# Optimization experiments

Hardware: AMD Instinct MI355X
Metric: run time of the kernel (lower is better)

Reference implementation:

```python
import jax, jax.numpy as jnp
import numpy as np

# Single-device reference: with head-parallel world size 1, both _SeqAllToAll
# collectives are identities, so the forward is exactly the kv-packed causal
# attention computed by loongtrain_attn_kvpacked_func (flash-attn semantics).

def setup_inputs() -> dict:
    key = jax.random.key(0)
    k1, k2 = jax.random.split(key)
    B, S, H, D = 1, 2048, 32, 128
    q = jax.random.normal(k1, (B, S, H, D), dtype=jnp.float32)
    kv = jax.random.normal(k2, (B, S, 2, H, D), dtype=jnp.float32)
    return {"q": q, "kv": kv}


def reference(q, kv) -> jnp.ndarray:
    # q: [B, S, H, D]; kv: [B, S, 2, H, D] (flash-attn kvpacked layout)
    B, S, H, D = q.shape
    k = kv[:, :, 0]  # [B, S, H, D]
    v = kv[:, :, 1]  # [B, S, H, D]
    scale = 1.0 / jnp.sqrt(jnp.asarray(D, dtype=q.dtype))
    # scores: [B, H, Sq, Sk]
    scores = jnp.einsum("bshd,bthd->bhst", q, k) * scale
    # causal mask (LoongTrain attention is causal)
    causal = jnp.tril(jnp.ones((S, S), dtype=bool))
    scores = jnp.where(causal[None, None, :, :], scores, jnp.asarray(-jnp.inf, dtype=scores.dtype))
    probs = jax.nn.softmax(scores, axis=-1)
    # context: [B, S, H, D]
    context = jnp.einsum("bhst,bthd->bshd", probs, v)
    return context
```

## Files before the change

### kernel.cpp

```cpp
#include <hip/hip_runtime.h>
#include <hip/hip_bf16.h>

typedef __bf16 bf16_t;
typedef __bf16 bf16x4 __attribute__((ext_vector_type(4)));
typedef __bf16 bf16x8 __attribute__((ext_vector_type(8)));
typedef float  f32x4  __attribute__((ext_vector_type(4)));

constexpr int S  = 2048;
constexpr int H  = 32;
constexpr int D  = 128;
constexpr int BR = 128;
constexpr int SC = 32;
constexpr int NT = S / BR;
constexpr int KSTR  = 136;
constexpr int VSTR2 = 20;
constexpr int PSTR  = 40;

__device__ __forceinline__ bf16x8 cvt8(f32x4 lo, f32x4 hi) {
    bf16x8 r;
#pragma unroll
    for (int j = 0; j < 4; ++j) { r[j] = (bf16_t)lo[j]; r[4 + j] = (bf16_t)hi[j]; }
    return r;
}
__device__ __forceinline__ uint32_t pk2(float a, float b) {
    union { uint32_t u; bf16_t h[2]; } r;
    r.h[0] = (bf16_t)a; r.h[1] = (bf16_t)b;
    return r.u;
}

__global__ __launch_bounds__(256, 2)
void fa_fwd(const float* __restrict__ q, const float* __restrict__ kvp,
            float* __restrict__ out) {
    __shared__ __align__(16) bf16_t   Klds[2][SC * KSTR];
    __shared__ __align__(16) uint32_t Vt2[2][D * VSTR2];
    __shared__ __align__(16) bf16_t   PT[4 * 32 * PSTR];

    const int bx = blockIdx.x;
    const int h  = bx & 31;
    const int i  = bx >> 5;
    const int qtile = (i < 8) ? (15 - i) : (i - 8);
    const int q0    = qtile * BR;

    const int t    = threadIdx.x;
    const int w    = t >> 6;
    const int lane = t & 63;
    const int quad = lane >> 4;
    const int m    = lane & 15;

    const float sc = 0.08838834764831845f * 1.44269504088896340f;

    const int k2 = t >> 4, kc = t & 15;
    const size_t rowstep = (size_t)2 * H * D;
    const size_t tstep   = (size_t)SC * rowstep;
    const float* pk = kvp + (((size_t)(2 * k2) * 2 + 0) * H + h) * D + kc * 8;
    const float* pv = kvp + (((size_t)(2 * k2) * 2 + 1) * H + h) * D + kc * 8;
    const int vpos = k2 ^ ((kc & 3) << 2);
    bf16_t* PTw = &PT[w * 32 * PSTR];

    const int qp0   = q0 + w * 32 + m;
    const int nkv   = (qtile + 1) * (BR / SC);
    const int qmaxw = q0 + w * 32 + 31;

    bf16x8 aq[2][4];
#pragma unroll
    for (int g = 0; g < 2; ++g)
#pragma unroll
        for (int c = 0; c < 4; ++c) {
            const float* p = q + ((size_t)(qp0 + g * 16) * H + h) * D + c * 32 + quad * 8;
            f32x4 lo = *(const f32x4*)p * sc;
            f32x4 hi = *(const f32x4*)(p + 4) * sc;
            aq[g][c] = cvt8(lo, hi);
        }

    f32x4 o[2][8];
#pragma unroll
    for (int g = 0; g < 2; ++g)
#pragma unroll
        for (int idx = 0; idx < 8; ++idx) o[g][idx] = (f32x4)0.f;
    float lrow[2] = {0.f, 0.f};

    f32x4 kr[2][2], vr[2][2];
    auto ldregs = [&]() {
        kr[0][0] = *(const f32x4*)pk;             kr[0][1] = *(const f32x4*)(pk + 4);
        kr[1][0] = *(const f32x4*)(pk + rowstep); kr[1][1] = *(const f32x4*)(pk + rowstep + 4);
        vr[0][0] = *(const f32x4*)pv;             vr[0][1] = *(const f32x4*)(pv + 4);
        vr[1][0] = *(const f32x4*)(pv + rowstep); vr[1][1] = *(const f32x4*)(pv + rowstep + 4);
    };
    auto stage = [&](int b) {
        *(bf16x8*)&Klds[b][(2 * k2)     * KSTR + kc * 8] = cvt8(kr[0][0], kr[0][1]);
        *(bf16x8*)&Klds[b][(2 * k2 + 1) * KSTR + kc * 8] = cvt8(kr[1][0], kr[1][1]);
#pragma unroll
        for (int j = 0; j < 8; ++j) {
            const int d = kc * 8 + j;
            const float a  = (j < 4) ? vr[0][0][j] : vr[0][1][j - 4];
            const float bb = (j < 4) ? vr[1][0][j] : vr[1][1][j - 4];
            Vt2[b][d * VSTR2 + vpos] = pk2(a, bb);
        }
    };

    ldregs();
    stage(0);
    if (nkv > 1) { pk += tstep; pv += tstep; ldregs(); }
    __syncthreads();

    for (int kb = 0; kb < nkv; ++kb) {
        const int kv0 = kb * SC;
        const int cur = kb & 1;
        const bool active = (kv0 <= qmaxw);

        bf16x8 bp0, bp1, av[8];
        if (active) {
            f32x4 sA[2][2];
#pragma unroll
            for (int g = 0; g < 2; ++g) { sA[g][0] = (f32x4)0.f; sA[g][1] = (f32x4)0.f; }
#pragma unroll
            for (int c = 0; c < 4; ++c) {
                bf16x8 ak0 = *(const bf16x8*)&Klds[cur][m * KSTR + c * 32 + quad * 8];
                bf16x8 ak1 = *(const bf16x8*)&Klds[cur][(16 + m) * KSTR + c * 32 + quad * 8];
                sA[0][0] = __builtin_amdgcn_mfma_f32_16x16x32_bf16(ak0, aq[0][c], sA[0][0], 0, 0, 0);
                sA[0][1] = __builtin_amdgcn_mfma_f32_16x16x32_bf16(ak1, aq[0][c], sA[0][1], 0, 0, 0);
                sA[1][0] = __builtin_amdgcn_mfma_f32_16x16x32_bf16(ak0, aq[1][c], sA[1][0], 0, 0, 0);
                sA[1][1] = __builtin_amdgcn_mfma_f32_16x16x32_bf16(ak1, aq[1][c], sA[1][1], 0, 0, 0);
            }

#pragma unroll
            for (int g = 0; g < 2; ++g) {
                const int lim = (qp0 + g * 16) - kv0;
                float p[8], rs = 0.f;
#pragma unroll
                for (int r = 0; r < 4; ++r) {
                    float e0 = __builtin_amdgcn_exp2f(fminf(sA[g][0][r], 80.f));
                    float e1 = __builtin_amdgcn_exp2f(fminf(sA[g][1][r], 80.f));
                    p[r]     = (quad * 4 + r      <= lim) ? e0 : 0.f;
                    p[4 + r] = (16 + quad * 4 + r <= lim) ? e1 : 0.f;
                    rs += p[r] + p[4 + r];
                }
                lrow[g] += rs;
                bf16x4 pa, pb;
#pragma unroll
                for (int r = 0; r < 4; ++r) { pa[r] = (bf16_t)p[r]; pb[r] = (bf16_t)p[4 + r]; }
                *(bf16x4*)&PTw[(g * 16 + m) * PSTR + quad * 4]      = pa;
                *(bf16x4*)&PTw[(g * 16 + m) * PSTR + 16 + quad * 4] = pb;
            }
            asm volatile("s_waitcnt lgkmcnt(0)" ::: "memory");
            bp0 = *(const bf16x8*)&PTw[m * PSTR + quad * 8];
            bp1 = *(const bf16x8*)&PTw[(16 + m) * PSTR + quad * 8];
#pragma unroll
            for (int tt = 0; tt < 8; ++tt) {
                const int dd  = tt * 16 + m;
                const int grp = quad ^ ((dd >> 3) & 3);
                av[tt] = *(const bf16x8*)&Vt2[cur][dd * VSTR2 + grp * 4];
            }
        }

        if (kb + 1 < nkv) {
            stage(cur ^ 1);
            if (kb + 2 < nkv) { pk += tstep; pv += tstep; ldregs(); }
        }

        if (active) {
#pragma unroll
            for (int tt = 0; tt < 8; ++tt) {
                o[0][tt] = __builtin_amdgcn_mfma_f32_16x16x32_bf16(av[tt], bp0, o[0][tt], 0, 0, 0);
                o[1][tt] = __builtin_amdgcn_mfma_f32_16x16x32_bf16(av[tt], bp1, o[1][tt], 0, 0, 0);
            }
        }
        __syncthreads();
    }

#pragma unroll
    for (int g = 0; g < 2; ++g) {
        lrow[g] += __shfl_xor(lrow[g], 16);
        lrow[g] += __shfl_xor(lrow[g], 32);
    }

#pragma unroll
    for (int g = 0; g < 2; ++g) {
        const float inv = 1.0f / lrow[g];
        float* op = out + ((size_t)(qp0 + g * 16) * H + h) * D;
#pragma unroll
        for (int tt = 0; tt < 8; ++tt) {
            f32x4 val = o[g][tt] * inv;
            *(f32x4*)(op + tt * 16 + quad * 4) = val;
        }
    }
}

extern "C" void kernel_launch(void* const* d_in, const int* in_sizes, int n_in,
                              void* d_out, int out_size, void* d_ws, size_t ws_size,
                              hipStream_t stream) {
    const float* q  = (const float*)d_in[0];
    const float* kv = (const float*)d_in[1];
    float* out = (float*)d_out;
    dim3 grid(NT * H);
    dim3 block(256);
    fa_fwd<<<grid, block, 0, stream>>>(q, kv, out);
}
```

Measured before the change: 180.2 us.

## Permute K rows in LDS so P stays in registers, skip P LDS round-trip

Permutes the order in which K rows are written into shared memory so that the QK^T MFMA output layout for each lane matches the B-operand layout needed by the PV MFMA. The probability tile can then be packed into bf16x8 registers directly, with no write to and read back from a per-wave LDS buffer, which removes that LDS traffic, a wait and some shared memory. It also adds a fast path that skips causal-mask compares for fully unmasked tiles, and raises wave priority around the MFMA blocks with s_setprio. The risk is that the row permutation must stay consistent with the V layout and the mask index math.

```diff
diff --git a/kernel.cpp b/kernel.cpp
--- a/kernel.cpp
+++ b/kernel.cpp
@@ -14,7 +14,6 @@
 constexpr int NT = S / BR;
 constexpr int KSTR  = 136;
 constexpr int VSTR2 = 20;
-constexpr int PSTR  = 40;
 
 __device__ __forceinline__ bf16x8 cvt8(f32x4 lo, f32x4 hi) {
     bf16x8 r;
@@ -33,7 +32,6 @@
             float* __restrict__ out) {
     __shared__ __align__(16) bf16_t   Klds[2][SC * KSTR];
     __shared__ __align__(16) uint32_t Vt2[2][D * VSTR2];
-    __shared__ __align__(16) bf16_t   PT[4 * 32 * PSTR];
 
     const int bx = blockIdx.x;
     const int h  = bx & 31;
@@ -50,12 +48,13 @@
     const float sc = 0.08838834764831845f * 1.44269504088896340f;
 
     const int k2 = t >> 4, kc = t & 15;
+    const int r0 = 2 * k2;
+    const int lr0 = ((r0 >> 3) << 2) + (r0 & 3) + ((r0 & 4) ? 16 : 0);
     const size_t rowstep = (size_t)2 * H * D;
     const size_t tstep   = (size_t)SC * rowstep;
-    const float* pk = kvp + (((size_t)(2 * k2) * 2 + 0) * H + h) * D + kc * 8;
-    const float* pv = kvp + (((size_t)(2 * k2) * 2 + 1) * H + h) * D + kc * 8;
+    const float* pk = kvp + (((size_t)r0 * 2 + 0) * H + h) * D + kc * 8;
+    const float* pv = kvp + (((size_t)r0 * 2 + 1) * H + h) * D + kc * 8;
     const int vpos = k2 ^ ((kc & 3) << 2);
-    bf16_t* PTw = &PT[w * 32 * PSTR];
 
     const int qp0   = q0 + w * 32 + m;
     const int nkv   = (qtile + 1) * (BR / SC);
@@ -87,8 +86,8 @@
         vr[1][0] = *(const f32x4*)(pv + rowstep); vr[1][1] = *(const f32x4*)(pv + rowstep + 4);
     };
     auto stage = [&](int b) {
-        *(bf16x8*)&Klds[b][(2 * k2)     * KSTR + kc * 8] = cvt8(kr[0][0], kr[0][1]);
-        *(bf16x8*)&Klds[b][(2 * k2 + 1) * KSTR + kc * 8] = cvt8(kr[1][0], kr[1][1]);
+        *(bf16x8*)&Klds[b][lr0       * KSTR + kc * 8] = cvt8(kr[0][0], kr[0][1]);
+        *(bf16x8*)&Klds[b][(lr0 + 1) * KSTR + kc * 8] = cvt8(kr[1][0], kr[1][1]);
 #pragma unroll
         for (int j = 0; j < 8; ++j) {
             const int d = kc * 8 + j;
@@ -113,6 +112,7 @@
             f32x4 sA[2][2];
 #pragma unroll
             for (int g = 0; g < 2; ++g) { sA[g][0] = (f32x4)0.f; sA[g][1] = (f32x4)0.f; }
+            __builtin_amdgcn_s_setprio(1);
 #pragma unroll
             for (int c = 0; c < 4; ++c) {
                 bf16x8 ak0 = *(const bf16x8*)&Klds[cur][m * KSTR + c * 32 + quad * 8];
@@ -122,35 +122,43 @@
                 sA[1][0] = __builtin_amdgcn_mfma_f32_16x16x32_bf16(ak0, aq[1][c], sA[1][0], 0, 0, 0);
                 sA[1][1] = __builtin_amdgcn_mfma_f32_16x16x32_bf16(ak1, aq[1][c], sA[1][1], 0, 0, 0);
             }
-
-#pragma unroll
-            for (int g = 0; g < 2; ++g) {
-                const int lim = (qp0 + g * 16) - kv0;
-                float p[8], rs = 0.f;
-#pragma unroll
-                for (int r = 0; r < 4; ++r) {
-                    float e0 = __builtin_amdgcn_exp2f(fminf(sA[g][0][r], 80.f));
-                    float e1 = __builtin_amdgcn_exp2f(fminf(sA[g][1][r], 80.f));
-                    p[r]     = (quad * 4 + r      <= lim) ? e0 : 0.f;
-                    p[4 + r] = (16 + quad * 4 + r <= lim) ? e1 : 0.f;
-                    rs += p[r] + p[4 + r];
-                }
-                lrow[g] += rs;
-                bf16x4 pa, pb;
-#pragma unroll
-                for (int r = 0; r < 4; ++r) { pa[r] = (bf16_t)p[r]; pb[r] = (bf16_t)p[4 + r]; }
-                *(bf16x4*)&PTw[(g * 16 + m) * PSTR + quad * 4]      = pa;
-                *(bf16x4*)&PTw[(g * 16 + m) * PSTR + 16 + quad * 4] = pb;
-            }
-            asm volatile("s_waitcnt lgkmcnt(0)" ::: "memory");
-            bp0 = *(const bf16x8*)&PTw[m * PSTR + quad * 8];
-            bp1 = *(const bf16x8*)&PTw[(16 + m) * PSTR + quad * 8];
+            __builtin_amdgcn_s_setprio(0);
+
 #pragma unroll
             for (int tt = 0; tt < 8; ++tt) {
                 const int dd  = tt * 16 + m;
                 const int grp = quad ^ ((dd >> 3) & 3);
                 av[tt] = *(const bf16x8*)&Vt2[cur][dd * VSTR2 + grp * 4];
             }
+
+#pragma unroll
+            for (int g = 0; g < 2; ++g) {
+                const int limb = q0 + w * 32 + g * 16 - kv0;
+                float p[8], rs = 0.f;
+                if (limb >= 31) {
+#pragma unroll
+                    for (int r = 0; r < 4; ++r) {
+                        p[r]     = __builtin_amdgcn_exp2f(fminf(sA[g][0][r], 80.f));
+                        p[4 + r] = __builtin_amdgcn_exp2f(fminf(sA[g][1][r], 80.f));
+                        rs += p[r] + p[4 + r];
+                    }
+                } else {
+                    const int lim = limb + m;
+#pragma unroll
+                    for (int r = 0; r < 4; ++r) {
+                        float e0 = __builtin_amdgcn_exp2f(fminf(sA[g][0][r], 80.f));
+                        float e1 = __builtin_amdgcn_exp2f(fminf(sA[g][1][r], 80.f));
+                        p[r]     = (quad * 8 + r     <= lim) ? e0 : 0.f;
+                        p[4 + r] = (quad * 8 + 4 + r <= lim) ? e1 : 0.f;
+                        rs += p[r] + p[4 + r];
+                    }
+                }
+                lrow[g] += rs;
+                bf16x8 bv;
+#pragma unroll
+                for (int r = 0; r < 4; ++r) { bv[r] = (bf16_t)p[r]; bv[4 + r] = (bf16_t)p[4 + r]; }
+                if (g == 0) bp0 = bv; else bp1 = bv;
+            }
         }
 
         if (kb + 1 < nkv) {
@@ -159,11 +167,13 @@
         }
 
         if (active) {
+            __builtin_amdgcn_s_setprio(1);
 #pragma unroll
             for (int tt = 0; tt < 8; ++tt) {
                 o[0][tt] = __builtin_amdgcn_mfma_f32_16x16x32_bf16(av[tt], bp0, o[0][tt], 0, 0, 0);
                 o[1][tt] = __builtin_amdgcn_mfma_f32_16x16x32_bf16(av[tt], bp1, o[1][tt], 0, 0, 0);
             }
+            __builtin_amdgcn_s_setprio(0);
         }
         __syncthreads();
     }
```

Result: no change. 176.9 us (-1.8%).
